# Optimization experiments

Measured on AMD Instinct MI355X. Metric: run time of the kernel, lower is better.

## Reference

```python
import jax, jax.numpy as jnp
import numpy as np

EMBED_DIM = 1024
B, S = 4, 2048


def setup_inputs() -> dict:
    key = jax.random.key(0)
    ks = jax.random.split(key, 7)
    D = EMBED_DIM
    lim = 1.0 / np.sqrt(D)  # torch nn.Linear default init range
    inp = {
        "input": jax.random.normal(ks[0], (B, S, D), dtype=jnp.float32),
        "Wq": jax.random.uniform(ks[1], (D, D), jnp.float32, -lim, lim),
        "bq": jax.random.uniform(ks[2], (D,), jnp.float32, -lim, lim),
        "Wk": jax.random.uniform(ks[3], (D, D), jnp.float32, -lim, lim),
        "bk": jax.random.uniform(ks[4], (D,), jnp.float32, -lim, lim),
        "Wv": jax.random.uniform(ks[5], (D, D), jnp.float32, -lim, lim),
        "bv": jax.random.uniform(ks[6], (D,), jnp.float32, -lim, lim),
    }
    return inp


def reference(input, Wq, bq, Wk, bk, Wv, bv):
    # Linear layers: x @ W^T + b (torch convention: W is [out, in])
    q = jnp.einsum("bsd,ed->bse", input, Wq) + bq
    k = jnp.einsum("bsd,ed->bse", input, Wk) + bk
    v = jnp.einsum("bsd,ed->bse", input, Wv) + bv
    scale = 1.0 / jnp.sqrt(jnp.float32(EMBED_DIM))
    # [B, S, S] similarity matrix (unfused, matches original)
    similarity = jnp.einsum("bqd,bkd->bqk", q, k) * scale
    attention = jax.nn.softmax(similarity, axis=-1)
    return jnp.einsum("bqk,bkd->bqd", attention, v)
```

## Files before the change

kernel.cpp:

```cpp
#include <hip/hip_runtime.h>


typedef unsigned short ushort_t;
typedef __bf16 bf16x8 __attribute__((ext_vector_type(8)));
typedef float f32x4 __attribute__((ext_vector_type(4)));
typedef _Float16 h8 __attribute__((ext_vector_type(8)));
typedef short short8v __attribute__((ext_vector_type(8)));

__device__ __forceinline__ unsigned short f2bf(float f) {
  unsigned u = __builtin_bit_cast(unsigned, f);
  u += 0x7fffu + ((u >> 16) & 1u);
  return (unsigned short)(u >> 16);
}

template<int MODE, int RX, int RY>
__global__ __launch_bounds__(512, 4)
void gemm128(const ushort_t* __restrict__ A, long long sAz, int lda,
             const ushort_t* __restrict__ Bm, long long sBz, int ldb,
             void* __restrict__ C0, void* __restrict__ C1, void* __restrict__ C2,
             long long sCz, int ldc, int K, float scale, const float* __restrict__ bias)
{
  constexpr int SLOT = 8192;
  constexpr int BUF  = 2 * SLOT;
  __shared__ ushort_t lds_[2 * BUF] __attribute__((aligned(16)));

  constexpr int BPR = RX * RY;
  const int gx = gridDim.x;
  const int lin = blockIdx.y * gx + blockIdx.x;
  const int xcd = lin & 7, s = lin >> 3;
  const int chunk = s / BPR, idx = s % BPR;
  const int rect = chunk * 8 + xcd;
  const int nrx = gx / RX;
  const int bx = (rect % nrx) * RX + (idx % RX);
  const int by = (rect / nrx) * RY + (idx / RX);

  const int z = blockIdx.z;
  const ushort_t* Ab = A  + (long long)z * sAz + (long long)by * 128 * lda;
  const ushort_t* Bb = Bm + (long long)z * sBz + (long long)bx * 128 * ldb;

  const int tid = threadIdx.x, wid = tid >> 6, lane = tid & 63;
  const int wr = wid >> 2, wc = wid & 3;
  const int l15 = lane & 15;
  const int kx0 = (((lane >> 4) + 0) ^ (l15 & 7)) * 8;
  const int kx1 = (((lane >> 4) + 4) ^ (l15 & 7)) * 8;
  const int srow = lane >> 3;
  const int scol = ((lane & 7) ^ (srow & 7)) * 8;

  const ushort_t* agA = Ab + (long long)(wid * 8 + srow) * lda + scol;
  const ushort_t* agB = Bb + (long long)(wid * 8 + srow) * ldb + scol;
  const long long jA = (long long)64 * lda, jB = (long long)64 * ldb;
  const int ldsA0 = wid * 512;
  const int ldsB0 = SLOT + wid * 512;

  auto stage = [&](const ushort_t* g, long long jstep, int ldsOff) {
#pragma unroll
    for (int j = 0; j < 2; ++j)
      __builtin_amdgcn_global_load_lds(
          (const __attribute__((address_space(1))) void*)(g + j * jstep),
          (__attribute__((address_space(3))) void*)(&lds_[ldsOff + j * 4096]),
          16, 0, 0);
  };

  f32x4 acc[4][2];
#pragma unroll
  for (int m = 0; m < 4; ++m)
#pragma unroll
    for (int n = 0; n < 2; ++n)
#pragma unroll
      for (int j = 0; j < 4; ++j) acc[m][n][j] = 0.f;

  stage(agA, jA, 0 * BUF + ldsA0); agA += 64;
  stage(agB, jB, 0 * BUF + ldsB0); agB += 64;
  stage(agA, jA, 1 * BUF + ldsA0); agA += 64;
  stage(agB, jB, 1 * BUF + ldsB0); agB += 64;
  asm volatile("s_waitcnt vmcnt(4)" ::: "memory");
  __builtin_amdgcn_s_barrier();

  const int NT = K >> 6;
  bf16x8 a0[4], a1[4], bf[2];

  for (int t = 0; t < NT; ++t) {
    const int q = t & 1;
    const ushort_t* Al = &lds_[q * BUF] + wr * 4096;
    const ushort_t* Bl = &lds_[q * BUF + SLOT] + wc * 2048;

#pragma unroll
    for (int m = 0; m < 4; ++m) a0[m] = *(const bf16x8*)(Al + (m * 16 + l15) * 64 + kx0);
#pragma unroll
    for (int n = 0; n < 2; ++n) bf[n] = *(const bf16x8*)(Bl + (n * 16 + l15) * 64 + kx0);
#pragma unroll
    for (int m = 0; m < 4; ++m) a1[m] = *(const bf16x8*)(Al + (m * 16 + l15) * 64 + kx1);
    __builtin_amdgcn_s_barrier();
    __builtin_amdgcn_s_setprio(1);
#pragma unroll
    for (int m = 0; m < 4; ++m)
#pragma unroll
      for (int n = 0; n < 2; ++n)
        acc[m][n] = __builtin_amdgcn_mfma_f32_16x16x32_bf16(a0[m], bf[n], acc[m][n], 0, 0, 0);
    __builtin_amdgcn_s_setprio(0);
    __builtin_amdgcn_s_barrier();

#pragma unroll
    for (int n = 0; n < 2; ++n) bf[n] = *(const bf16x8*)(Bl + (n * 16 + l15) * 64 + kx1);
    asm volatile("s_waitcnt lgkmcnt(0)" ::: "memory");
    __builtin_amdgcn_sched_barrier(0);
    if (t + 2 < NT) {
      stage(agA, jA, q * BUF + ldsA0); agA += 64;
      stage(agB, jB, q * BUF + ldsB0); agB += 64;
    }
    __builtin_amdgcn_s_barrier();
    __builtin_amdgcn_s_setprio(1);
#pragma unroll
    for (int m = 0; m < 4; ++m)
#pragma unroll
      for (int n = 0; n < 2; ++n)
        acc[m][n] = __builtin_amdgcn_mfma_f32_16x16x32_bf16(a1[m], bf[n], acc[m][n], 0, 0, 0);
    __builtin_amdgcn_s_setprio(0);
    if (t < NT - 2)       asm volatile("s_waitcnt vmcnt(4)" ::: "memory");
    else if (t == NT - 2) asm volatile("s_waitcnt vmcnt(0)" ::: "memory");
    __builtin_amdgcn_s_barrier();
  }

  const int r4 = (lane >> 4) * 4;
  const long long crow0 = (long long)by * 128 + wr * 64;
  const int ccol0 = bx * 128 + wc * 32;

  if constexpr (MODE == 0) {
#pragma unroll
    for (int n = 0; n < 2; ++n) {
      const int cg = ccol0 + n * 16 + l15;
#pragma unroll
      for (int m = 0; m < 4; ++m)
#pragma unroll
        for (int j = 0; j < 4; ++j) {
          const long long rg = crow0 + m * 16 + r4 + j;
          ((float*)C0)[(long long)z * sCz + rg * ldc + cg] = acc[m][n][j] * scale;
        }
    }
  } else {
    const int sel = ccol0 >> 10;
#pragma unroll
    for (int n = 0; n < 2; ++n) {
      const int cg = ccol0 + n * 16 + l15;
      const int col = cg & 1023;
      const float badd = bias[cg];
      if (sel < 2) {
        ushort_t* outp = (ushort_t*)(sel == 0 ? C0 : C1);
#pragma unroll
        for (int m = 0; m < 4; ++m)
#pragma unroll
          for (int j = 0; j < 4; ++j) {
            const long long rg = crow0 + m * 16 + r4 + j;
            outp[rg * 1024 + col] = f2bf(acc[m][n][j] + badd);
          }
      } else {
        ushort_t* vt = (ushort_t*)C2;
#pragma unroll
        for (int m = 0; m < 4; ++m) {
          const long long rg = crow0 + m * 16 + r4;
          const long long b = rg >> 11, srw = rg & 2047;
          ushort4 o;
          o.x = f2bf(acc[m][n][0] + badd);
          o.y = f2bf(acc[m][n][1] + badd);
          o.z = f2bf(acc[m][n][2] + badd);
          o.w = f2bf(acc[m][n][3] + badd);
          *(ushort4*)&vt[b * 2097152 + (long long)col * 2048 + srw] = o;
        }
      }
    }
  }
}

__global__ __launch_bounds__(512, 1)
void gemm256(const ushort_t* __restrict__ A, long long sAz, int lda,
             const ushort_t* __restrict__ Bm, long long sBz, int ldb,
             _Float16* __restrict__ C, long long sCz, int ldc,
             int K, float scale)
{
  constexpr int AH = 8192, BH = 8192, BUF = 2 * AH + 2 * BH;
  constexpr int RX = 4, RY = 2, BPR = RX * RY;
  __shared__ ushort_t lds_[2 * BUF] __attribute__((aligned(16)));

  const int gx = gridDim.x;
  const int lin = blockIdx.y * gx + blockIdx.x;
  const int xcd = lin & 7, s = lin >> 3;
  const int chunk = s / BPR, idx = s % BPR;
  const int rect = chunk * 8 + xcd;
  const int nrx = gx / RX;
  const int bx = (rect % nrx) * RX + (idx % RX);
  const int by = (rect / nrx) * RY + (idx / RX);

  const int z = blockIdx.z;
  const ushort_t* Ab = A  + (long long)z * sAz + (long long)by * 256 * lda;
  const ushort_t* Bb = Bm + (long long)z * sBz + (long long)bx * 256 * ldb;

  const int tid = threadIdx.x, wid = tid >> 6, lane = tid & 63;
  const int wr = wid >> 2, wc = wid & 3;
  const int l15 = lane & 15;
  const int kx0 = (((lane >> 4) + 0) ^ (l15 & 7)) * 8;
  const int kx1 = (((lane >> 4) + 4) ^ (l15 & 7)) * 8;
  const int srow = lane >> 3;
  const int scol = ((lane & 7) ^ (srow & 7)) * 8;

  const ushort_t* agA = Ab + (long long)(wid * 16 + srow) * lda + scol;
  const ushort_t* agB = Bb + (long long)(wid * 16 + srow) * ldb + scol;

  auto stageA = [&](int q) {
#pragma unroll
    for (int h = 0; h < 2; ++h)
#pragma unroll
      for (int j = 0; j < 2; ++j)
        __builtin_amdgcn_global_load_lds(
            (const __attribute__((address_space(1))) void*)(agA + (long long)(h * 128 + j * 8) * lda),
            (__attribute__((address_space(3))) void*)
              (&lds_[q * BUF + h * AH + (wid * 128 + j * 64) * 8]),
            16, 0, 0);
  };
  auto stageB = [&](int q) {
#pragma unroll
    for (int h = 0; h < 2; ++h)
#pragma unroll
      for (int j = 0; j < 2; ++j)
        __builtin_amdgcn_global_load_lds(
            (const __attribute__((address_space(1))) void*)(agB + (long long)(h * 128 + j * 8) * ldb),
            (__attribute__((address_space(3))) void*)
              (&lds_[q * BUF + 2 * AH + h * BH + (wid * 128 + j * 64) * 8]),
            16, 0, 0);
  };

  f32x4 acc[8][4];
#pragma unroll
  for (int m = 0; m < 8; ++m)
#pragma unroll
    for (int n = 0; n < 4; ++n)
#pragma unroll
      for (int j = 0; j < 4; ++j) acc[m][n][j] = 0.f;

  stageA(0); stageB(0); agA += 64; agB += 64;
  stageA(1); stageB(1); agA += 64; agB += 64;
  asm volatile("s_waitcnt vmcnt(8)" ::: "memory");
  __builtin_amdgcn_s_barrier();

  const int NT = K >> 6;
  bf16x8 af[4], bf[4];

  for (int t = 0; t < NT; ++t) {
    const int q = t & 1;
    const ushort_t* Al = &lds_[q * BUF + wr * AH];
    const ushort_t* Bl = &lds_[q * BUF + 2 * AH + (wc >> 1) * BH + (wc & 1) * 4096];

#pragma unroll
    for (int n = 0; n < 4; ++n) bf[n] = *(const bf16x8*)(Bl + (n * 16 + l15) * 64 + kx0);
#pragma unroll
    for (int m = 0; m < 4; ++m) af[m] = *(const bf16x8*)(Al + (m * 16 + l15) * 64 + kx0);
    __builtin_amdgcn_s_barrier();
    __builtin_amdgcn_s_setprio(1);
#pragma unroll
    for (int m = 0; m < 4; ++m)
#pragma unroll
      for (int n = 0; n < 4; ++n)
        acc[m][n] = __builtin_amdgcn_mfma_f32_16x16x32_bf16(af[m], bf[n], acc[m][n], 0, 0, 0);
    __builtin_amdgcn_s_setprio(0);
    __builtin_amdgcn_s_barrier();

#pragma unroll
    for (int m = 0; m < 4; ++m) af[m] = *(const bf16x8*)(Al + ((4 + m) * 16 + l15) * 64 + kx0);
    __builtin_amdgcn_s_barrier();
    __builtin_amdgcn_s_setprio(1);
#pragma unroll
    for (int m = 0; m < 4; ++m)
#pragma unroll
      for (int n = 0; n < 4; ++n)
        acc[4 + m][n] = __builtin_amdgcn_mfma_f32_16x16x32_bf16(af[m], bf[n], acc[4 + m][n], 0, 0, 0);
    __builtin_amdgcn_s_setprio(0);
    __builtin_amdgcn_s_barrier();

#pragma unroll
    for (int n = 0; n < 4; ++n) bf[n] = *(const bf16x8*)(Bl + (n * 16 + l15) * 64 + kx1);
#pragma unroll
    for (int m = 0; m < 4; ++m) af[m] = *(const bf16x8*)(Al + (m * 16 + l15) * 64 + kx1);
    __builtin_amdgcn_s_barrier();
    __builtin_amdgcn_s_setprio(1);
#pragma unroll
    for (int m = 0; m < 4; ++m)
#pragma unroll
      for (int n = 0; n < 4; ++n)
        acc[m][n] = __builtin_amdgcn_mfma_f32_16x16x32_bf16(af[m], bf[n], acc[m][n], 0, 0, 0);
    __builtin_amdgcn_s_setprio(0);
    __builtin_amdgcn_s_barrier();

#pragma unroll
    for (int m = 0; m < 4; ++m) af[m] = *(const bf16x8*)(Al + ((4 + m) * 16 + l15) * 64 + kx1);
    asm volatile("s_waitcnt lgkmcnt(0)" ::: "memory");
    __builtin_amdgcn_sched_barrier(0);
    if (t + 2 < NT) { stageA(q); stageB(q); agA += 64; agB += 64; }
    __builtin_amdgcn_s_barrier();
    __builtin_amdgcn_s_setprio(1);
#pragma unroll
    for (int m = 0; m < 4; ++m)
#pragma unroll
      for (int n = 0; n < 4; ++n)
        acc[4 + m][n] = __builtin_amdgcn_mfma_f32_16x16x32_bf16(af[m], bf[n], acc[4 + m][n], 0, 0, 0);
    __builtin_amdgcn_s_setprio(0);
    if (t < NT - 2)       asm volatile("s_waitcnt vmcnt(8)" ::: "memory");
    else if (t == NT - 2) asm volatile("s_waitcnt vmcnt(0)" ::: "memory");
    __builtin_amdgcn_s_barrier();
  }

  const int r4 = (lane >> 4) * 4;
  const long long crow0 = (long long)by * 256 + wr * 128;
  const int ccol0 = bx * 256 + wc * 64;
#pragma unroll
  for (int n = 0; n < 4; ++n) {
    const int cg = ccol0 + n * 16 + l15;
#pragma unroll
    for (int m = 0; m < 8; ++m)
#pragma unroll
      for (int j = 0; j < 4; ++j) {
        const long long rg = crow0 + m * 16 + r4 + j;
        C[(long long)z * sCz + rg * ldc + cg] = (_Float16)(acc[m][n][j] * scale);
      }
  }
}

__global__ __launch_bounds__(256)
void cast_f32_bf16(const float* __restrict__ in, ushort_t* __restrict__ out, long long n)
{
  long long i = ((long long)blockIdx.x * blockDim.x + threadIdx.x) * 4;
  const long long stride = (long long)gridDim.x * blockDim.x * 4;
  for (; i < n; i += stride) {
    const float4 v = *(const float4*)&in[i];
    ushort4 o;
    o.x = f2bf(v.x); o.y = f2bf(v.y); o.z = f2bf(v.z); o.w = f2bf(v.w);
    *(ushort4*)&out[i] = o;
  }
}

__global__ __launch_bounds__(256)
void prep_w(const float* __restrict__ Wq, const float* __restrict__ Wk,
            const float* __restrict__ Wv, const float* __restrict__ bq,
            const float* __restrict__ bk, const float* __restrict__ bv,
            ushort_t* __restrict__ w3, float* __restrict__ bcat)
{
  const int which = blockIdx.x >> 10;
  const float* W = (which == 0) ? Wq : (which == 1) ? Wk : Wv;
  const long long i = ((long long)(blockIdx.x & 1023) * 256 + threadIdx.x) * 4;
  const float4 v = *(const float4*)&W[i];
  ushort4 o;
  o.x = f2bf(v.x); o.y = f2bf(v.y); o.z = f2bf(v.z); o.w = f2bf(v.w);
  *(ushort4*)&w3[(long long)which * 1024 * 1024 + i] = o;
  const int g = blockIdx.x * 256 + threadIdx.x;
  if (g < 3072) bcat[g] = (g < 1024) ? bq[g] : (g < 2048) ? bk[g - 1024] : bv[g - 2048];
}

__global__ __launch_bounds__(256)
void softmax2048(const _Float16* __restrict__ Sc, ushort_t* __restrict__ P)
{
  const long long row = blockIdx.x;
  const _Float16* s = Sc + row * 2048;
  const int tid = threadIdx.x;
  const int wave = tid >> 6, lane = tid & 63;

  const h8 a = *(const h8*)&s[tid * 8];
  float f[8];
#pragma unroll
  for (int i = 0; i < 8; ++i) f[i] = (float)a[i];
  float m = fmaxf(fmaxf(fmaxf(f[0], f[1]), fmaxf(f[2], f[3])),
                  fmaxf(fmaxf(f[4], f[5]), fmaxf(f[6], f[7])));
#pragma unroll
  for (int off = 32; off > 0; off >>= 1) m = fmaxf(m, __shfl_xor(m, off));
  __shared__ float redm[4], reds[4];
  if (lane == 0) redm[wave] = m;
  __syncthreads();
  m = fmaxf(fmaxf(redm[0], redm[1]), fmaxf(redm[2], redm[3]));

  float e[8];
#pragma unroll
  for (int i = 0; i < 8; ++i) e[i] = __expf(f[i] - m);
  float sum = ((e[0] + e[1]) + (e[2] + e[3])) + ((e[4] + e[5]) + (e[6] + e[7]));
#pragma unroll
  for (int off = 32; off > 0; off >>= 1) sum += __shfl_xor(sum, off);
  if (lane == 0) reds[wave] = sum;
  __syncthreads();
  sum = (reds[0] + reds[1]) + (reds[2] + reds[3]);
  const float inv = 1.0f / sum;

  short8v o;
#pragma unroll
  for (int i = 0; i < 8; ++i) o[i] = (short)f2bf(e[i] * inv);
  *(short8v*)&P[row * 2048 + tid * 8] = o;
}

extern "C" void kernel_launch(void* const* d_in, const int* in_sizes, int n_in,
                              void* d_out, int out_size, void* d_ws, size_t ws_size,
                              hipStream_t stream)
{
  constexpr int B = 4, S = 2048, D = 1024;
  constexpr long long MT = (long long)B * S;
  constexpr long long SD = (long long)S * D;
  constexpr long long SS = (long long)S * S;

  const float* x  = (const float*)d_in[0];
  const float* Wq = (const float*)d_in[1];
  const float* bq = (const float*)d_in[2];
  const float* Wk = (const float*)d_in[3];
  const float* bk = (const float*)d_in[4];
  const float* Wv = (const float*)d_in[5];
  const float* bv = (const float*)d_in[6];
  float* out = (float*)d_out;

  char* base = (char*)d_ws;
  ushort_t*  q       = (ushort_t*)(base);
  ushort_t*  k       = (ushort_t*)(base + 16777216);
  ushort_t*  vt      = (ushort_t*)(base + 33554432);
  _Float16*  scores  = (_Float16*)(base + 50331648);
  ushort_t*  P       = (ushort_t*)(base + 117440512);
  ushort_t*  xb      = (ushort_t*)(base + 83886080);
  ushort_t*  w3      = (ushort_t*)(base + 100663296);
  float*     bcat    = (float*)   (base + 106954752);

  cast_f32_bf16<<<2048, 256, 0, stream>>>(x, xb, MT * D);
  prep_w<<<3072, 256, 0, stream>>>(Wq, Wk, Wv, bq, bk, bv, w3, bcat);

  gemm128<2, 4, 8><<<dim3(24, 64, 1), 512, 0, stream>>>(
      xb, 0, D, w3, 0, D, q, k, vt, 0, 1024, D, 1.f, bcat);

  gemm256<<<dim3(8, 8, 4), 512, 0, stream>>>(
      q, SD, D, k, SD, D, scores, SS, S, D, 0.03125f);

  softmax2048<<<MT, 256, 0, stream>>>(scores, P);

  gemm128<0, 2, 4><<<dim3(8, 16, 4), 512, 0, stream>>>(
      P, SS, S, vt, (long long)D * S, S, out, nullptr, nullptr, SD, D, S, 1.f, nullptr);
}
```

Before: 168.6 us.

## Replace projection GEMM with simpler 256-thread kernel using 64x64 warp tiles

Adds a dedicated projection GEMM with 256 threads and 4 waves. Each wave computes a 64x64 tile with 4x4 MFMA accumulators and loads a single-buffered 128x64 K-slice directly from global to LDS. The aim is more MFMA reuse per LDS fragment load than the 512-thread double-buffered kernel, at the cost of giving up load/compute pipelining. The remaining gemm128 specialisation is renamed to a PV-only kernel and the unused scale multiply is dropped.

```diff
diff --git a/kernel.cpp b/kernel.cpp
--- a/kernel.cpp
+++ b/kernel.cpp
@@ -13,12 +13,115 @@
   return (unsigned short)(u >> 16);
 }
 
-template<int MODE, int RX, int RY>
+__global__ __launch_bounds__(256, 4)
+void proj_gemm(const ushort_t* __restrict__ A, int lda,
+               const ushort_t* __restrict__ Bm, int ldb,
+               ushort_t* __restrict__ Cq, ushort_t* __restrict__ Ck,
+               ushort_t* __restrict__ Cvt, int K,
+               const float* __restrict__ bias)
+{
+  __shared__ ushort_t smA[128 * 64] __attribute__((aligned(16)));
+  __shared__ ushort_t smB[128 * 64] __attribute__((aligned(16)));
+
+  constexpr int RX = 4, RY = 8, BPR = RX * RY;
+  const int gx = gridDim.x;
+  const int lin = blockIdx.y * gx + blockIdx.x;
+  const int xcd = lin & 7, s = lin >> 3;
+  const int chunk = s / BPR, idx = s % BPR;
+  const int rect = chunk * 8 + xcd;
+  const int nrx = gx / RX;
+  const int bx = (rect % nrx) * RX + (idx % RX);
+  const int by = (rect / nrx) * RY + (idx / RX);
+
+  const int row0 = by * 128, col0 = bx * 128;
+
+  const int tid = threadIdx.x;
+  const int wave = tid >> 6, lane = tid & 63;
+  const int wr = (wave >> 1) * 64, wc = (wave & 1) * 64;
+  const int l15 = lane & 15;
+
+  const int srow = tid >> 3;
+  const int scol = ((tid & 7) ^ (srow & 7)) * 8;
+  const ushort_t* ag = A  + (long long)(row0 + srow) * lda + scol;
+  const ushort_t* bg = Bm + (long long)(col0 + srow) * ldb + scol;
+  ushort_t* ldsA = &smA[(wave * 8) * 64];
+  ushort_t* ldsB = &smB[(wave * 8) * 64];
+
+  f32x4 acc[4][4];
+#pragma unroll
+  for (int m = 0; m < 4; ++m)
+#pragma unroll
+    for (int n = 0; n < 4; ++n)
+#pragma unroll
+      for (int j = 0; j < 4; ++j) acc[m][n][j] = 0.f;
+
+  for (int k0 = 0; k0 < K; k0 += 64) {
+#pragma unroll
+    for (int i = 0; i < 4; ++i) {
+      __builtin_amdgcn_global_load_lds(
+          (const __attribute__((address_space(1))) void*)(ag + (long long)i * 32 * lda + k0),
+          (__attribute__((address_space(3))) void*)(ldsA + i * 32 * 64), 16, 0, 0);
+      __builtin_amdgcn_global_load_lds(
+          (const __attribute__((address_space(1))) void*)(bg + (long long)i * 32 * ldb + k0),
+          (__attribute__((address_space(3))) void*)(ldsB + i * 32 * 64), 16, 0, 0);
+    }
+    __syncthreads();
+#pragma unroll
+    for (int kk = 0; kk < 2; ++kk) {
+      const int kx = (((lane >> 4) + 4 * kk) ^ (l15 & 7)) * 8;
+      bf16x8 af[4], bfv[4];
+#pragma unroll
+      for (int m = 0; m < 4; ++m)
+        af[m] = *(const bf16x8*)&smA[(wr + m * 16 + l15) * 64 + kx];
+#pragma unroll
+      for (int n = 0; n < 4; ++n)
+        bfv[n] = *(const bf16x8*)&smB[(wc + n * 16 + l15) * 64 + kx];
+#pragma unroll
+      for (int m = 0; m < 4; ++m)
+#pragma unroll
+        for (int n = 0; n < 4; ++n)
+          acc[m][n] = __builtin_amdgcn_mfma_f32_16x16x32_bf16(af[m], bfv[n], acc[m][n], 0, 0, 0);
+    }
+    __syncthreads();
+  }
+
+  const int r4 = (lane >> 4) * 4;
+  const int sel = col0 >> 10;
+#pragma unroll
+  for (int n = 0; n < 4; ++n) {
+    const int cg = col0 + wc + n * 16 + l15;
+    const int col = cg & 1023;
+    const float badd = bias[cg];
+    if (sel < 2) {
+      ushort_t* outp = (sel == 0) ? Cq : Ck;
+#pragma unroll
+      for (int m = 0; m < 4; ++m)
+#pragma unroll
+        for (int j = 0; j < 4; ++j) {
+          const long long rg = row0 + wr + m * 16 + r4 + j;
+          outp[rg * 1024 + col] = f2bf(acc[m][n][j] + badd);
+        }
+    } else {
+#pragma unroll
+      for (int m = 0; m < 4; ++m) {
+        const long long rg = row0 + wr + m * 16 + r4;
+        const long long b = rg >> 11, srw = rg & 2047;
+        ushort4 o;
+        o.x = f2bf(acc[m][n][0] + badd);
+        o.y = f2bf(acc[m][n][1] + badd);
+        o.z = f2bf(acc[m][n][2] + badd);
+        o.w = f2bf(acc[m][n][3] + badd);
+        *(ushort4*)&Cvt[b * 2097152 + (long long)col * 2048 + srw] = o;
+      }
+    }
+  }
+}
+
+template<int RX, int RY>
 __global__ __launch_bounds__(512, 4)
-void gemm128(const ushort_t* __restrict__ A, long long sAz, int lda,
+void pv_gemm(const ushort_t* __restrict__ A, long long sAz, int lda,
              const ushort_t* __restrict__ Bm, long long sBz, int ldb,
-             void* __restrict__ C0, void* __restrict__ C1, void* __restrict__ C2,
-             long long sCz, int ldc, int K, float scale, const float* __restrict__ bias)
+             float* __restrict__ C0, long long sCz, int ldc, int K)
 {
   constexpr int SLOT = 8192;
   constexpr int BUF  = 2 * SLOT;
@@ -124,55 +227,21 @@
   const int r4 = (lane >> 4) * 4;
   const long long crow0 = (long long)by * 128 + wr * 64;
   const int ccol0 = bx * 128 + wc * 32;
-
-  if constexpr (MODE == 0) {
-#pragma unroll
-    for (int n = 0; n < 2; ++n) {
-      const int cg = ccol0 + n * 16 + l15;
-#pragma unroll
-      for (int m = 0; m < 4; ++m)
-#pragma unroll
-        for (int j = 0; j < 4; ++j) {
-          const long long rg = crow0 + m * 16 + r4 + j;
-          ((float*)C0)[(long long)z * sCz + rg * ldc + cg] = acc[m][n][j] * scale;
-        }
-    }
-  } else {
-    const int sel = ccol0 >> 10;
-#pragma unroll
-    for (int n = 0; n < 2; ++n) {
-      const int cg = ccol0 + n * 16 + l15;
-      const int col = cg & 1023;
-      const float badd = bias[cg];
-      if (sel < 2) {
-        ushort_t* outp = (ushort_t*)(sel == 0 ? C0 : C1);
-#pragma unroll
-        for (int m = 0; m < 4; ++m)
-#pragma unroll
-          for (int j = 0; j < 4; ++j) {
-            const long long rg = crow0 + m * 16 + r4 + j;
-            outp[rg * 1024 + col] = f2bf(acc[m][n][j] + badd);
-          }
-      } else {
-        ushort_t* vt = (ushort_t*)C2;
-#pragma unroll
-        for (int m = 0; m < 4; ++m) {
-          const long long rg = crow0 + m * 16 + r4;
-          const long long b = rg >> 11, srw = rg & 2047;
-          ushort4 o;
-          o.x = f2bf(acc[m][n][0] + badd);
-          o.y = f2bf(acc[m][n][1] + badd);
-          o.z = f2bf(acc[m][n][2] + badd);
-          o.w = f2bf(acc[m][n][3] + badd);
-          *(ushort4*)&vt[b * 2097152 + (long long)col * 2048 + srw] = o;
-        }
+#pragma unroll
+  for (int n = 0; n < 2; ++n) {
+    const int cg = ccol0 + n * 16 + l15;
+#pragma unroll
+    for (int m = 0; m < 4; ++m)
+#pragma unroll
+      for (int j = 0; j < 4; ++j) {
+        const long long rg = crow0 + m * 16 + r4 + j;
+        C0[(long long)z * sCz + rg * ldc + cg] = acc[m][n][j];
       }
-    }
   }
 }
 
 __global__ __launch_bounds__(512, 1)
-void gemm256(const ushort_t* __restrict__ A, long long sAz, int lda,
+void qk_gemm(const ushort_t* __restrict__ A, long long sAz, int lda,
              const ushort_t* __restrict__ Bm, long long sBz, int ldb,
              _Float16* __restrict__ C, long long sCz, int ldc,
              int K, float scale)
@@ -422,14 +491,14 @@
   cast_f32_bf16<<<2048, 256, 0, stream>>>(x, xb, MT * D);
   prep_w<<<3072, 256, 0, stream>>>(Wq, Wk, Wv, bq, bk, bv, w3, bcat);
 
-  gemm128<2, 4, 8><<<dim3(24, 64, 1), 512, 0, stream>>>(
-      xb, 0, D, w3, 0, D, q, k, vt, 0, 1024, D, 1.f, bcat);
-
-  gemm256<<<dim3(8, 8, 4), 512, 0, stream>>>(
+  proj_gemm<<<dim3(24, 64, 1), 256, 0, stream>>>(
+      xb, D, w3, D, q, k, vt, D, bcat);
+
+  qk_gemm<<<dim3(8, 8, 4), 512, 0, stream>>>(
       q, SD, D, k, SD, D, scores, SS, S, D, 0.03125f);
 
   softmax2048<<<MT, 256, 0, stream>>>(scores, P);
 
-  gemm128<0, 2, 4><<<dim3(8, 16, 4), 512, 0, stream>>>(
-      P, SS, S, vt, (long long)D * S, S, out, nullptr, nullptr, SD, D, S, 1.f, nullptr);
-}
+  pv_gemm<2, 4><<<dim3(8, 16, 4), 512, 0, stream>>>(
+      P, SS, S, vt, (long long)D * S, S, out, SD, D, S);
+}
```

Measured after the change: 164.3 us. -2.5%, faster.

## Replace QKV and QK^T GEMMs with a 256x256 four-stage ring-buffered GEMM

Applied to the files above, without the earlier changes.

Introduces a ring_gemm kernel that uses 256x256 output tiles with a K-step of 32 and a 4-deep LDS ring buffer, issuing loads three steps ahead and using a single barrier per iteration. It replaces both the 128-tile QKV projection GEMM and the separate 256-tile QK^T GEMM, while the PV GEMM keeps the old 128-tile double-buffered design under a new name. The aim is deeper prefetch and fewer barriers. In exchange, the new LDS layout has no XOR swizzle, so fragment reads may hit bank conflicts, and the QKV grid shrinks to 384 blocks at one block per CU.

```diff
diff --git a/kernel.cpp b/kernel.cpp
--- a/kernel.cpp
+++ b/kernel.cpp
@@ -14,15 +14,16 @@
 }
 
 template<int MODE, int RX, int RY>
-__global__ __launch_bounds__(512, 4)
-void gemm128(const ushort_t* __restrict__ A, long long sAz, int lda,
-             const ushort_t* __restrict__ Bm, long long sBz, int ldb,
-             void* __restrict__ C0, void* __restrict__ C1, void* __restrict__ C2,
-             long long sCz, int ldc, int K, float scale, const float* __restrict__ bias)
-{
-  constexpr int SLOT = 8192;
-  constexpr int BUF  = 2 * SLOT;
-  __shared__ ushort_t lds_[2 * BUF] __attribute__((aligned(16)));
+__global__ __launch_bounds__(512, 1)
+void ring_gemm(const ushort_t* __restrict__ A, long long sAz, int lda,
+               const ushort_t* __restrict__ Bm, long long sBz, int ldb,
+               void* __restrict__ C0, void* __restrict__ C1, void* __restrict__ C2,
+               long long sCz, int ldc, int K, float scale,
+               const float* __restrict__ bias)
+{
+  constexpr int ABUF = 256 * 32;
+  constexpr int TBUF = 2 * ABUF;
+  __shared__ ushort_t lds_[4 * TBUF] __attribute__((aligned(16)));
 
   constexpr int BPR = RX * RY;
   const int gx = gridDim.x;
@@ -35,119 +36,104 @@
   const int by = (rect / nrx) * RY + (idx / RX);
 
   const int z = blockIdx.z;
-  const ushort_t* Ab = A  + (long long)z * sAz + (long long)by * 128 * lda;
-  const ushort_t* Bb = Bm + (long long)z * sBz + (long long)bx * 128 * ldb;
+  const ushort_t* Ab = A  + (long long)z * sAz + (long long)by * 256 * lda;
+  const ushort_t* Bb = Bm + (long long)z * sBz + (long long)bx * 256 * ldb;
 
   const int tid = threadIdx.x, wid = tid >> 6, lane = tid & 63;
   const int wr = wid >> 2, wc = wid & 3;
   const int l15 = lane & 15;
-  const int kx0 = (((lane >> 4) + 0) ^ (l15 & 7)) * 8;
-  const int kx1 = (((lane >> 4) + 4) ^ (l15 & 7)) * 8;
-  const int srow = lane >> 3;
-  const int scol = ((lane & 7) ^ (srow & 7)) * 8;
-
-  const ushort_t* agA = Ab + (long long)(wid * 8 + srow) * lda + scol;
-  const ushort_t* agB = Bb + (long long)(wid * 8 + srow) * ldb + scol;
-  const long long jA = (long long)64 * lda, jB = (long long)64 * ldb;
-  const int ldsA0 = wid * 512;
-  const int ldsB0 = SLOT + wid * 512;
-
-  auto stage = [&](const ushort_t* g, long long jstep, int ldsOff) {
-#pragma unroll
-    for (int j = 0; j < 2; ++j)
+  const int kq = (lane >> 4) * 8;
+
+  const int srow = lane >> 2;
+  const int scol = (lane & 3) * 8;
+  const ushort_t* agA = Ab + (long long)(wid * 32 + srow) * lda + scol;
+  const ushort_t* agB = Bb + (long long)(wid * 32 + srow) * ldb + scol;
+
+  auto stage = [&](int t) {
+    const int rb = (t & 3) * TBUF;
+#pragma unroll
+    for (int j = 0; j < 2; ++j) {
       __builtin_amdgcn_global_load_lds(
-          (const __attribute__((address_space(1))) void*)(g + j * jstep),
-          (__attribute__((address_space(3))) void*)(&lds_[ldsOff + j * 4096]),
+          (const __attribute__((address_space(1))) void*)(agA + (long long)(j * 16) * lda + t * 32),
+          (__attribute__((address_space(3))) void*)(&lds_[rb + (wid * 32 + j * 16) * 32]),
           16, 0, 0);
+      __builtin_amdgcn_global_load_lds(
+          (const __attribute__((address_space(1))) void*)(agB + (long long)(j * 16) * ldb + t * 32),
+          (__attribute__((address_space(3))) void*)(&lds_[rb + ABUF + (wid * 32 + j * 16) * 32]),
+          16, 0, 0);
+    }
   };
 
-  f32x4 acc[4][2];
-#pragma unroll
-  for (int m = 0; m < 4; ++m)
-#pragma unroll
-    for (int n = 0; n < 2; ++n)
+  f32x4 acc[8][4];
+#pragma unroll
+  for (int m = 0; m < 8; ++m)
+#pragma unroll
+    for (int n = 0; n < 4; ++n)
 #pragma unroll
       for (int j = 0; j < 4; ++j) acc[m][n][j] = 0.f;
 
-  stage(agA, jA, 0 * BUF + ldsA0); agA += 64;
-  stage(agB, jB, 0 * BUF + ldsB0); agB += 64;
-  stage(agA, jA, 1 * BUF + ldsA0); agA += 64;
-  stage(agB, jB, 1 * BUF + ldsB0); agB += 64;
-  asm volatile("s_waitcnt vmcnt(4)" ::: "memory");
+  const int NT = K >> 5;
+
+  stage(0); stage(1); stage(2);
+  asm volatile("s_waitcnt vmcnt(8)" ::: "memory");
   __builtin_amdgcn_s_barrier();
-
-  const int NT = K >> 6;
-  bf16x8 a0[4], a1[4], bf[2];
-
+  __builtin_amdgcn_sched_barrier(0);
+
+  bf16x8 af[8], bf[4];
   for (int t = 0; t < NT; ++t) {
-    const int q = t & 1;
-    const ushort_t* Al = &lds_[q * BUF] + wr * 4096;
-    const ushort_t* Bl = &lds_[q * BUF + SLOT] + wc * 2048;
-
-#pragma unroll
-    for (int m = 0; m < 4; ++m) a0[m] = *(const bf16x8*)(Al + (m * 16 + l15) * 64 + kx0);
-#pragma unroll
-    for (int n = 0; n < 2; ++n) bf[n] = *(const bf16x8*)(Bl + (n * 16 + l15) * 64 + kx0);
-#pragma unroll
-    for (int m = 0; m < 4; ++m) a1[m] = *(const bf16x8*)(Al + (m * 16 + l15) * 64 + kx1);
-    __builtin_amdgcn_s_barrier();
+    if (t + 3 < NT) stage(t + 3);
+    __builtin_amdgcn_sched_barrier(0);
+
+    const ushort_t* Al = &lds_[(t & 3) * TBUF] + (wr * 128) * 32;
+    const ushort_t* Bl = &lds_[(t & 3) * TBUF + ABUF] + (wc * 64) * 32;
+#pragma unroll
+    for (int m = 0; m < 8; ++m) af[m] = *(const bf16x8*)(Al + (m * 16 + l15) * 32 + kq);
+#pragma unroll
+    for (int n = 0; n < 4; ++n) bf[n] = *(const bf16x8*)(Bl + (n * 16 + l15) * 32 + kq);
+
     __builtin_amdgcn_s_setprio(1);
 #pragma unroll
-    for (int m = 0; m < 4; ++m)
-#pragma unroll
-      for (int n = 0; n < 2; ++n)
-        acc[m][n] = __builtin_amdgcn_mfma_f32_16x16x32_bf16(a0[m], bf[n], acc[m][n], 0, 0, 0);
+    for (int m = 0; m < 8; ++m)
+#pragma unroll
+      for (int n = 0; n < 4; ++n)
+        acc[m][n] = __builtin_amdgcn_mfma_f32_16x16x32_bf16(af[m], bf[n], acc[m][n], 0, 0, 0);
     __builtin_amdgcn_s_setprio(0);
-    __builtin_amdgcn_s_barrier();
-
-#pragma unroll
-    for (int n = 0; n < 2; ++n) bf[n] = *(const bf16x8*)(Bl + (n * 16 + l15) * 64 + kx1);
-    asm volatile("s_waitcnt lgkmcnt(0)" ::: "memory");
+
+    if (t < NT - 3)       asm volatile("s_waitcnt vmcnt(8)" ::: "memory");
+    else if (t == NT - 3) asm volatile("s_waitcnt vmcnt(4)" ::: "memory");
+    else if (t == NT - 2) asm volatile("s_waitcnt vmcnt(0)" ::: "memory");
+    __builtin_amdgcn_s_barrier();
     __builtin_amdgcn_sched_barrier(0);
-    if (t + 2 < NT) {
-      stage(agA, jA, q * BUF + ldsA0); agA += 64;
-      stage(agB, jB, q * BUF + ldsB0); agB += 64;
-    }
-    __builtin_amdgcn_s_barrier();
-    __builtin_amdgcn_s_setprio(1);
-#pragma unroll
-    for (int m = 0; m < 4; ++m)
-#pragma unroll
-      for (int n = 0; n < 2; ++n)
-        acc[m][n] = __builtin_amdgcn_mfma_f32_16x16x32_bf16(a1[m], bf[n], acc[m][n], 0, 0, 0);
-    __builtin_amdgcn_s_setprio(0);
-    if (t < NT - 2)       asm volatile("s_waitcnt vmcnt(4)" ::: "memory");
-    else if (t == NT - 2) asm volatile("s_waitcnt vmcnt(0)" ::: "memory");
-    __builtin_amdgcn_s_barrier();
   }
 
   const int r4 = (lane >> 4) * 4;
-  const long long crow0 = (long long)by * 128 + wr * 64;
-  const int ccol0 = bx * 128 + wc * 32;
-
-  if constexpr (MODE == 0) {
-#pragma unroll
-    for (int n = 0; n < 2; ++n) {
+  const long long crow0 = (long long)by * 256 + wr * 128;
+  const int ccol0 = bx * 256 + wc * 64;
+
+  if constexpr (MODE == 1) {
+    _Float16* C = (_Float16*)C0;
+#pragma unroll
+    for (int n = 0; n < 4; ++n) {
       const int cg = ccol0 + n * 16 + l15;
 #pragma unroll
-      for (int m = 0; m < 4; ++m)
+      for (int m = 0; m < 8; ++m)
 #pragma unroll
         for (int j = 0; j < 4; ++j) {
           const long long rg = crow0 + m * 16 + r4 + j;
-          ((float*)C0)[(long long)z * sCz + rg * ldc + cg] = acc[m][n][j] * scale;
+          C[(long long)z * sCz + rg * ldc + cg] = (_Float16)(acc[m][n][j] * scale);
         }
     }
   } else {
     const int sel = ccol0 >> 10;
 #pragma unroll
-    for (int n = 0; n < 2; ++n) {
+    for (int n = 0; n < 4; ++n) {
       const int cg = ccol0 + n * 16 + l15;
       const int col = cg & 1023;
       const float badd = bias[cg];
       if (sel < 2) {
         ushort_t* outp = (ushort_t*)(sel == 0 ? C0 : C1);
 #pragma unroll
-        for (int m = 0; m < 4; ++m)
+        for (int m = 0; m < 8; ++m)
 #pragma unroll
           for (int j = 0; j < 4; ++j) {
             const long long rg = crow0 + m * 16 + r4 + j;
@@ -156,7 +142,7 @@
       } else {
         ushort_t* vt = (ushort_t*)C2;
 #pragma unroll
-        for (int m = 0; m < 4; ++m) {
+        for (int m = 0; m < 8; ++m) {
           const long long rg = crow0 + m * 16 + r4;
           const long long b = rg >> 11, srw = rg & 2047;
           ushort4 o;
@@ -171,16 +157,17 @@
   }
 }
 
-__global__ __launch_bounds__(512, 1)
-void gemm256(const ushort_t* __restrict__ A, long long sAz, int lda,
+template<int RX, int RY>
+__global__ __launch_bounds__(512, 4)
+void pv_gemm(const ushort_t* __restrict__ A, long long sAz, int lda,
              const ushort_t* __restrict__ Bm, long long sBz, int ldb,
-             _Float16* __restrict__ C, long long sCz, int ldc,
-             int K, float scale)
-{
-  constexpr int AH = 8192, BH = 8192, BUF = 2 * AH + 2 * BH;
-  constexpr int RX = 4, RY = 2, BPR = RX * RY;
+             float* __restrict__ C0, long long sCz, int ldc, int K)
+{
+  constexpr int SLOT = 8192;
+  constexpr int BUF  = 2 * SLOT;
   __shared__ ushort_t lds_[2 * BUF] __attribute__((aligned(16)));
 
+  constexpr int BPR = RX * RY;
   const int gx = gridDim.x;
   const int lin = blockIdx.y * gx + blockIdx.x;
   const int xcd = lin & 7, s = lin >> 3;
@@ -191,8 +178,8 @@
   const int by = (rect / nrx) * RY + (idx / RX);
 
   const int z = blockIdx.z;
-  const ushort_t* Ab = A  + (long long)z * sAz + (long long)by * 256 * lda;
-  const ushort_t* Bb = Bm + (long long)z * sBz + (long long)bx * 256 * ldb;
+  const ushort_t* Ab = A  + (long long)z * sAz + (long long)by * 128 * lda;
+  const ushort_t* Bb = Bm + (long long)z * sBz + (long long)bx * 128 * ldb;
 
   const int tid = threadIdx.x, wid = tid >> 6, lane = tid & 63;
   const int wr = wid >> 2, wc = wid & 3;
@@ -202,123 +189,93 @@
   const int srow = lane >> 3;
   const int scol = ((lane & 7) ^ (srow & 7)) * 8;
 
-  const ushort_t* agA = Ab + (long long)(wid * 16 + srow) * lda + scol;
-  const ushort_t* agB = Bb + (long long)(wid * 16 + srow) * ldb + scol;
-
-  auto stageA = [&](int q) {
-#pragma unroll
-    for (int h = 0; h < 2; ++h)
-#pragma unroll
-      for (int j = 0; j < 2; ++j)
-        __builtin_amdgcn_global_load_lds(
-            (const __attribute__((address_space(1))) void*)(agA + (long long)(h * 128 + j * 8) * lda),
-            (__attribute__((address_space(3))) void*)
-              (&lds_[q * BUF + h * AH + (wid * 128 + j * 64) * 8]),
-            16, 0, 0);
+  const ushort_t* agA = Ab + (long long)(wid * 8 + srow) * lda + scol;
+  const ushort_t* agB = Bb + (long long)(wid * 8 + srow) * ldb + scol;
+  const long long jA = (long long)64 * lda, jB = (long long)64 * ldb;
+  const int ldsA0 = wid * 512;
+  const int ldsB0 = SLOT + wid * 512;
+
+  auto stage = [&](const ushort_t* g, long long jstep, int ldsOff) {
+#pragma unroll
+    for (int j = 0; j < 2; ++j)
+      __builtin_amdgcn_global_load_lds(
+          (const __attribute__((address_space(1))) void*)(g + j * jstep),
+          (__attribute__((address_space(3))) void*)(&lds_[ldsOff + j * 4096]),
+          16, 0, 0);
   };
-  auto stageB = [&](int q) {
-#pragma unroll
-    for (int h = 0; h < 2; ++h)
-#pragma unroll
-      for (int j = 0; j < 2; ++j)
-        __builtin_amdgcn_global_load_lds(
-            (const __attribute__((address_space(1))) void*)(agB + (long long)(h * 128 + j * 8) * ldb),
-            (__attribute__((address_space(3))) void*)
-              (&lds_[q * BUF + 2 * AH + h * BH + (wid * 128 + j * 64) * 8]),
-            16, 0, 0);
-  };
-
-  f32x4 acc[8][4];
-#pragma unroll
-  for (int m = 0; m < 8; ++m)
-#pragma unroll
-    for (int n = 0; n < 4; ++n)
+
+  f32x4 acc[4][2];
+#pragma unroll
+  for (int m = 0; m < 4; ++m)
+#pragma unroll
+    for (int n = 0; n < 2; ++n)
 #pragma unroll
       for (int j = 0; j < 4; ++j) acc[m][n][j] = 0.f;
 
-  stageA(0); stageB(0); agA += 64; agB += 64;
-  stageA(1); stageB(1); agA += 64; agB += 64;
-  asm volatile("s_waitcnt vmcnt(8)" ::: "memory");
+  stage(agA, jA, 0 * BUF + ldsA0); agA += 64;
+  stage(agB, jB, 0 * BUF + ldsB0); agB += 64;
+  stage(agA, jA, 1 * BUF + ldsA0); agA += 64;
+  stage(agB, jB, 1 * BUF + ldsB0); agB += 64;
+  asm volatile("s_waitcnt vmcnt(4)" ::: "memory");
   __builtin_amdgcn_s_barrier();
 
   const int NT = K >> 6;
-  bf16x8 af[4], bf[4];
+  bf16x8 a0[4], a1[4], bf[2];
 
   for (int t = 0; t < NT; ++t) {
     const int q = t & 1;
-    const ushort_t* Al = &lds_[q * BUF + wr * AH];
-    const ushort_t* Bl = &lds_[q * BUF + 2 * AH + (wc >> 1) * BH + (wc & 1) * 4096];
-
-#pragma unroll
-    for (int n = 0; n < 4; ++n) bf[n] = *(const bf16x8*)(Bl + (n * 16 + l15) * 64 + kx0);
-#pragma unroll
-    for (int m = 0; m < 4; ++m) af[m] = *(const bf16x8*)(Al + (m * 16 + l15) * 64 + kx0);
+    const ushort_t* Al = &lds_[q * BUF] + wr * 4096;
+    const ushort_t* Bl = &lds_[q * BUF + SLOT] + wc * 2048;
+
+#pragma unroll
+    for (int m = 0; m < 4; ++m) a0[m] = *(const bf16x8*)(Al + (m * 16 + l15) * 64 + kx0);
+#pragma unroll
+    for (int n = 0; n < 2; ++n) bf[n] = *(const bf16x8*)(Bl + (n * 16 + l15) * 64 + kx0);
+#pragma unroll
+    for (int m = 0; m < 4; ++m) a1[m] = *(const bf16x8*)(Al + (m * 16 + l15) * 64 + kx1);
     __builtin_amdgcn_s_barrier();
     __builtin_amdgcn_s_setprio(1);
 #pragma unroll
     for (int m = 0; m < 4; ++m)
 #pragma unroll
-      for (int n = 0; n < 4; ++n)
-        acc[m][n] = __builtin_amdgcn_mfma_f32_16x16x32_bf16(af[m], bf[n], acc[m][n], 0, 0, 0);
+      for (int n = 0; n < 2; ++n)
+        acc[m][n] = __builtin_amdgcn_mfma_f32_16x16x32_bf16(a0[m], bf[n], acc[m][n], 0, 0, 0);
     __builtin_amdgcn_s_setprio(0);
     __builtin_amdgcn_s_barrier();
 
 #pragma unroll
-    for (int m = 0; m < 4; ++m) af[m] = *(const bf16x8*)(Al + ((4 + m) * 16 + l15) * 64 + kx0);
-    __builtin_amdgcn_s_barrier();
-    __builtin_amdgcn_s_setprio(1);
-#pragma unroll
-    for (int m = 0; m < 4; ++m)
-#pragma unroll
-      for (int n = 0; n < 4; ++n)
-        acc[4 + m][n] = __builtin_amdgcn_mfma_f32_16x16x32_bf16(af[m], bf[n], acc[4 + m][n], 0, 0, 0);
-    __builtin_amdgcn_s_setprio(0);
-    __builtin_amdgcn_s_barrier();
-
-#pragma unroll
-    for (int n = 0; n < 4; ++n) bf[n] = *(const bf16x8*)(Bl + (n * 16 + l15) * 64 + kx1);
-#pragma unroll
-    for (int m = 0; m < 4; ++m) af[m] = *(const bf16x8*)(Al + (m * 16 + l15) * 64 + kx1);
-    __builtin_amdgcn_s_barrier();
-    __builtin_amdgcn_s_setprio(1);
-#pragma unroll
-    for (int m = 0; m < 4; ++m)
-#pragma unroll
-      for (int n = 0; n < 4; ++n)
-        acc[m][n] = __builtin_amdgcn_mfma_f32_16x16x32_bf16(af[m], bf[n], acc[m][n], 0, 0, 0);
-    __builtin_amdgcn_s_setprio(0);
-    __builtin_amdgcn_s_barrier();
-
-#pragma unroll
-    for (int m = 0; m < 4; ++m) af[m] = *(const bf16x8*)(Al + ((4 + m) * 16 + l15) * 64 + kx1);
+    for (int n = 0; n < 2; ++n) bf[n] = *(const bf16x8*)(Bl + (n * 16 + l15) * 64 + kx1);
     asm volatile("s_waitcnt lgkmcnt(0)" ::: "memory");
     __builtin_amdgcn_sched_barrier(0);
-    if (t + 2 < NT) { stageA(q); stageB(q); agA += 64; agB += 64; }
+    if (t + 2 < NT) {
+      stage(agA, jA, q * BUF + ldsA0); agA += 64;
+      stage(agB, jB, q * BUF + ldsB0); agB += 64;
+    }
     __builtin_amdgcn_s_barrier();
     __builtin_amdgcn_s_setprio(1);
 #pragma unroll
     for (int m = 0; m < 4; ++m)
 #pragma unroll
-      for (int n = 0; n < 4; ++n)
-        acc[4 + m][n] = __builtin_amdgcn_mfma_f32_16x16x32_bf16(af[m], bf[n], acc[4 + m][n], 0, 0, 0);
+      for (int n = 0; n < 2; ++n)
+        acc[m][n] = __builtin_amdgcn_mfma_f32_16x16x32_bf16(a1[m], bf[n], acc[m][n], 0, 0, 0);
     __builtin_amdgcn_s_setprio(0);
-    if (t < NT - 2)       asm volatile("s_waitcnt vmcnt(8)" ::: "memory");
+    if (t < NT - 2)       asm volatile("s_waitcnt vmcnt(4)" ::: "memory");
     else if (t == NT - 2) asm volatile("s_waitcnt vmcnt(0)" ::: "memory");
     __builtin_amdgcn_s_barrier();
   }
 
   const int r4 = (lane >> 4) * 4;
-  const long long crow0 = (long long)by * 256 + wr * 128;
-  const int ccol0 = bx * 256 + wc * 64;
-#pragma unroll
-  for (int n = 0; n < 4; ++n) {
+  const long long crow0 = (long long)by * 128 + wr * 64;
+  const int ccol0 = bx * 128 + wc * 32;
+#pragma unroll
+  for (int n = 0; n < 2; ++n) {
     const int cg = ccol0 + n * 16 + l15;
 #pragma unroll
-    for (int m = 0; m < 8; ++m)
+    for (int m = 0; m < 4; ++m)
 #pragma unroll
       for (int j = 0; j < 4; ++j) {
         const long long rg = crow0 + m * 16 + r4 + j;
-        C[(long long)z * sCz + rg * ldc + cg] = (_Float16)(acc[m][n][j] * scale);
+        C0[(long long)z * sCz + rg * ldc + cg] = acc[m][n][j];
       }
   }
 }
@@ -422,14 +379,14 @@
   cast_f32_bf16<<<2048, 256, 0, stream>>>(x, xb, MT * D);
   prep_w<<<3072, 256, 0, stream>>>(Wq, Wk, Wv, bq, bk, bv, w3, bcat);
 
-  gemm128<2, 4, 8><<<dim3(24, 64, 1), 512, 0, stream>>>(
+  ring_gemm<2, 4, 2><<<dim3(12, 32, 1), 512, 0, stream>>>(
       xb, 0, D, w3, 0, D, q, k, vt, 0, 1024, D, 1.f, bcat);
 
-  gemm256<<<dim3(8, 8, 4), 512, 0, stream>>>(
-      q, SD, D, k, SD, D, scores, SS, S, D, 0.03125f);
+  ring_gemm<1, 4, 2><<<dim3(8, 8, 4), 512, 0, stream>>>(
+      q, SD, D, k, SD, D, scores, nullptr, nullptr, SS, S, D, 0.03125f, nullptr);
 
   softmax2048<<<MT, 256, 0, stream>>>(scores, P);
 
-  gemm128<0, 2, 4><<<dim3(8, 16, 4), 512, 0, stream>>>(
-      P, SS, S, vt, (long long)D * S, S, out, nullptr, nullptr, SD, D, S, 1.f, nullptr);
-}
+  pv_gemm<2, 4><<<dim3(8, 16, 4), 512, 0, stream>>>(
+      P, SS, S, vt, (long long)D * S, S, out, SD, D, S);
+}
```

New measurement: 187.9 us. 1.11x slower.
